# Kernel tuning notes

Hardware: AMD Instinct MI355X
Metric: run time of the kernel (lower is better)

Reference implementation:

```python
import jax, jax.numpy as jnp
import numpy as np
import math

D_MODEL, D_STATE, N_LAYERS, D_CONV, EXPAND = 64, 16, 2, 4, 2
D_INNER = EXPAND * D_MODEL
DT_RANK = math.ceil(D_MODEL / 16)
B, N, T = 2, 16, 2048


def setup_inputs() -> dict:
    key = jax.random.key(0)
    ks = jax.random.split(key, 10)
    A_row = jnp.log(jnp.arange(1, D_STATE + 1, dtype=jnp.float32))  # S4D-real init
    return {
        "x": jax.random.normal(ks[0], (B, N, T), jnp.float32),
        "input_proj_w": jax.random.normal(ks[1], (D_MODEL, 1), jnp.float32) * 0.02,
        "input_proj_b": jnp.zeros((D_MODEL,), jnp.float32),
        "in_proj_w": jax.random.normal(ks[2], (N_LAYERS, 2 * D_INNER, D_MODEL), jnp.float32) * 0.02,
        "conv_w": jax.random.normal(ks[3], (N_LAYERS, D_INNER, 1, D_CONV), jnp.float32) * 0.1,
        "conv_b": jnp.zeros((N_LAYERS, D_INNER), jnp.float32),
        "x_proj_w": jax.random.normal(ks[4], (N_LAYERS, DT_RANK + 2 * D_STATE, D_INNER), jnp.float32) * 0.02,
        "dt_proj_w": jax.random.normal(ks[5], (N_LAYERS, D_INNER, DT_RANK), jnp.float32) * 0.1,
        "dt_proj_b": jax.random.normal(ks[6], (N_LAYERS, D_INNER), jnp.float32) * 0.02,
        "A_log": jnp.tile(A_row[None, None, :], (N_LAYERS, D_INNER, 1)),  # [L, d_inner, d_state]
        "D": jnp.ones((N_LAYERS, D_INNER), jnp.float32),
        "out_proj_w": jax.random.normal(ks[7], (N_LAYERS, D_MODEL, D_INNER), jnp.float32) * 0.02,
    }


def _silu(v):
    return v * jax.nn.sigmoid(v)


def _mamba_block(h, in_w, cw, cb, xw, dtw, dtb, A_log, Dp, ow):
    # h: [Bf, T, d_model]
    xr = jnp.einsum('btd,ed->bte', h, in_w)           # [Bf, T, 2*d_inner]
    x, res = jnp.split(xr, 2, axis=-1)                # each [Bf, T, d_inner]
    # causal depthwise conv1d (torch: padding=d_conv-1 then truncate to T)
    xc = jnp.transpose(x, (0, 2, 1))                  # [Bf, d_inner, T]
    xc = jax.lax.conv_general_dilated(xc, cw, (1,), [(D_CONV - 1, 0)],
                                      feature_group_count=D_INNER)
    x = _silu(jnp.transpose(xc, (0, 2, 1)) + cb[None, None, :])
    A = -jnp.exp(A_log)                               # [d_inner, d_state]
    x_dbl = jnp.einsum('btd,ed->bte', x, xw)          # [Bf, T, dt_rank+2*d_state]
    delta, Bm, Cm = jnp.split(x_dbl, [DT_RANK, DT_RANK + D_STATE], axis=-1)
    delta = jax.nn.softplus(jnp.einsum('btr,dr->btd', delta, dtw) + dtb)

    def step(hs, inp):
        d_t, B_t, C_t, u_t = inp                      # [Bf,d], [Bf,n], [Bf,n], [Bf,d]
        dA = jnp.exp(d_t[:, :, None] * A)             # [Bf, d, n]
        hs = dA * hs + (d_t * u_t)[:, :, None] * B_t[:, None, :]
        return hs, jnp.einsum('bdn,bn->bd', hs, C_t)

    xs = (jnp.swapaxes(delta, 0, 1), jnp.swapaxes(Bm, 0, 1),
          jnp.swapaxes(Cm, 0, 1), jnp.swapaxes(x, 0, 1))
    hs0 = jnp.zeros((h.shape[0], D_INNER, D_STATE), h.dtype)
    _, ys = jax.lax.scan(step, hs0, xs)               # ys: [T, Bf, d_inner]
    y = jnp.swapaxes(ys, 0, 1) + x * Dp[None, None, :]
    y = y * _silu(res)
    return jnp.einsum('btd,md->btm', y, ow) + h       # block residual


def reference(x, input_proj_w, input_proj_b, in_proj_w, conv_w, conv_b,
              x_proj_w, dt_proj_w, dt_proj_b, A_log, D, out_proj_w):
    b, n, t = x.shape
    h = x.reshape(b * n, t, 1)
    h = jnp.einsum('btk,dk->btd', h, input_proj_w) + input_proj_b
    for l in range(N_LAYERS):
        h = _mamba_block(h, in_proj_w[l], conv_w[l], conv_b[l], x_proj_w[l],
                         dt_proj_w[l], dt_proj_b[l], A_log[l], D[l], out_proj_w[l])
    return h.reshape(b, n, t, D_MODEL)
```

## Files before the change

kernel.cpp:

```cpp
#include <hip/hip_runtime.h>
#include <hip/hip_bf16.h>

#define BN     32
#define T      2048
#define DM     64
#define DI     128
#define DS     16
#define DTR    4
#define NLAY   2
#define RTOT   (BN*T)
#define NC     128
#define LC     (T/NC)

typedef float v2f __attribute__((ext_vector_type(2)));
typedef float f32x4 __attribute__((ext_vector_type(4)));
typedef __bf16 bf16x8 __attribute__((ext_vector_type(8)));
struct V22 { v2f a, b; };

__device__ __forceinline__ float silu_f(float v) {
    return v / (1.f + __expf(-v));
}
__device__ __forceinline__ unsigned short f2bf(float f) {
    __hip_bfloat16 b = __float2bfloat16(f);
    return __builtin_bit_cast(unsigned short, b);
}
__device__ __forceinline__ float bf_lo(unsigned int u) { return __uint_as_float(u << 16); }
__device__ __forceinline__ float bf_hi(unsigned int u) { return __uint_as_float(u & 0xffff0000u); }
__device__ __forceinline__ float us2f(unsigned short u) { return __uint_as_float(((unsigned)u) << 16); }
__device__ __forceinline__ void f4v2(const float4 f, v2f& a, v2f& b) {
    V22 u = __builtin_bit_cast(V22, f);
    a = u.a; b = u.b;
}
__device__ __forceinline__ float4 v2f4(v2f a, v2f b) {
    V22 u; u.a = a; u.b = b;
    return __builtin_bit_cast(float4, u);
}
__device__ __forceinline__ f32x4 mfma16(bf16x8 a, bf16x8 b, f32x4 c) {
    return __builtin_amdgcn_mfma_f32_16x16x32_bf16(a, b, c, 0, 0, 0);
}

#define E_POWERS2(e1, EE)                                              \
    float p2 = (e1)*(e1); float p4 = p2*p2; float p8 = p4*p4;          \
    v2f EE[8];                                                         \
    EE[0] = (v2f){(e1), p2};                                           \
    EE[1] = EE[0] * p2;                                                \
    EE[2] = EE[0] * p4;                                                \
    EE[3] = EE[1] * p4;                                                \
    EE[4] = EE[0] * p8;                                                \
    EE[5] = EE[1] * p8;                                                \
    EE[6] = EE[2] * p8;                                                \
    EE[7] = EE[3] * p8;

__global__ void k_initwt(const float* __restrict__ inw, const float* __restrict__ xw,
                         const float* __restrict__ ow, unsigned short* __restrict__ wti,
                         unsigned short* __restrict__ wtx, unsigned short* __restrict__ wto) {
    int i = blockIdx.x * 256 + threadIdx.x;
    if (i < 32768) {
        int l = i >> 14, pos = i & 16383;
        int j    = pos & 7;
        int lane = (pos >> 3) & 63;
        int ks   = (pos >> 9) & 1;
        int ct   = pos >> 10;
        int e = ct * 16 + (lane & 15);
        int k = ks * 32 + ((lane >> 4) & 3) * 8 + j;
        wti[l * 16384 + pos] = f2bf(inw[l * 16384 + e * 64 + k]);
    } else if (i < 45056) {
        int j = i - 32768;
        int l = (j >= 6144) ? 1 : 0;
        int pos = j - l * 6144;
        int jj   = pos & 7;
        int lane = (pos >> 3) & 63;
        int ks   = (pos >> 9) & 3;
        int ct   = pos >> 11;
        int m = ct * 16 + (lane & 15);
        int k = ks * 32 + ((lane >> 4) & 3) * 8 + jj;
        wtx[l * 6144 + pos] = (m < 36) ? f2bf(xw[l * 4608 + m * 128 + k])
                                       : (unsigned short)0;
    } else if (i < 61440) {
        int j = i - 45056;
        int l = j >> 13, pos = j & 8191;
        int jj   = pos & 7;
        int lane = (pos >> 3) & 63;
        int ks   = (pos >> 9) & 3;
        int ct   = pos >> 11;
        int m = ct * 16 + (lane & 15);
        int k = ks * 32 + ((lane >> 4) & 3) * 8 + jj;
        wto[l * 8192 + pos] = f2bf(ow[l * 8192 + m * 128 + k]);
    }
}

__global__ __launch_bounds__(256, 4)
void k_inconv(const float* __restrict__ hg, const float* __restrict__ xin,
              const float* __restrict__ ipw, const float* __restrict__ ipb,
              float* __restrict__ hout, const int L0,
              const unsigned short* __restrict__ wtiF,
              const float* __restrict__ cw, const float* __restrict__ cb,
              const unsigned short* __restrict__ wtxF,
              const float* __restrict__ dtw, const float* __restrict__ dtb,
              unsigned short* __restrict__ ubf, unsigned short* __restrict__ rbf,
              unsigned short* __restrict__ Hp, float* __restrict__ Sd) {
    __shared__ __align__(16) float smem[10112];
    unsigned short* A16 = (unsigned short*)smem;
    unsigned short* xub = A16 + 11520;
    float* xdbf = smem;

    const int tid  = threadIdx.x;
    const int base = blockIdx.x * 64;
    const int t0   = base & (T - 1);

#pragma unroll
    for (int k5 = 0; k5 < 5; ++k5) {
        int s = tid + k5 * 256;
        int i = s >> 4, q = s & 15;
        int lt = t0 - 16 + i;
        float4 v = make_float4(0.f, 0.f, 0.f, 0.f);
        if (lt >= 0) {
            int row = base - 16 + i;
            if (L0) {
                float xv = xin[row];
                float4 wq = *(const float4*)&ipw[q * 4];
                float4 bq = *(const float4*)&ipb[q * 4];
                v = make_float4(xv * wq.x + bq.x, xv * wq.y + bq.y,
                                xv * wq.z + bq.z, xv * wq.w + bq.w);
                if (i >= 16) *(float4*)&hout[(size_t)row * 64 + q * 4] = v;
            } else {
                v = *(const float4*)&hg[(size_t)row * 64 + q * 4];
            }
        }
        float vf[4] = {v.x, v.y, v.z, v.w};
        unsigned short hs[4], ls[4];
#pragma unroll
        for (int m = 0; m < 4; ++m) {
            hs[m] = f2bf(vf[m]);
            float hf = us2f(hs[m]);
            ls[m] = f2bf(vf[m] - hf);
        }
        unsigned int hw0 = (unsigned)hs[0] | ((unsigned)hs[1] << 16);
        unsigned int hw1 = (unsigned)hs[2] | ((unsigned)hs[3] << 16);
        unsigned int lw0 = (unsigned)ls[0] | ((unsigned)ls[1] << 16);
        unsigned int lw1 = (unsigned)ls[2] | ((unsigned)ls[3] << 16);
        *(uint2*)&A16[(size_t)i * 72 + q * 4]        = make_uint2(hw0, hw1);
        *(uint2*)&A16[(size_t)(80 + i) * 72 + q * 4] = make_uint2(lw0, lw1);
    }

    const int l  = tid & 63;
    const int w  = tid >> 6;
    const int lr = l & 15;
    const int lg = l >> 4;

    const uint4* bp = (const uint4*)wtiF;
    bf16x8 bfr[4][2];
#pragma unroll
    for (int ct = 0; ct < 4; ++ct)
#pragma unroll
        for (int ks = 0; ks < 2; ++ks)
            bfr[ct][ks] = __builtin_bit_cast(bf16x8, bp[(((w * 4 + ct) * 2 + ks) * 64) + l]);

    __syncthreads();

    f32x4 acc[5][4];
#pragma unroll
    for (int rt = 0; rt < 5; ++rt)
#pragma unroll
        for (int ct = 0; ct < 4; ++ct)
            acc[rt][ct] = (f32x4){0.f, 0.f, 0.f, 0.f};

#pragma unroll
    for (int rt = 0; rt < 5; ++rt) {
        if (rt == 0 && w >= 2) continue;
        bf16x8 ah[2], al[2];
#pragma unroll
        for (int ks = 0; ks < 2; ++ks) {
            int idx = (rt * 16 + lr) * 72 + ks * 32 + lg * 8;
            ah[ks] = __builtin_bit_cast(bf16x8, *(const uint4*)&A16[idx]);
            al[ks] = __builtin_bit_cast(bf16x8, *(const uint4*)&A16[80 * 72 + idx]);
        }
#pragma unroll
        for (int ct = 0; ct < 4; ++ct) {
#pragma unroll
            for (int ks = 0; ks < 2; ++ks) {
                acc[rt][ct] = mfma16(ah[ks], bfr[ct][ks], acc[rt][ct]);
                acc[rt][ct] = mfma16(al[ks], bfr[ct][ks], acc[rt][ct]);
            }
        }
    }

    if (w < 2) {
        const int srcl = (l + 48) & 63;
        float4 cwv[4]; float cbv[4];
#pragma unroll
        for (int ct = 0; ct < 4; ++ct) {
            int c = w * 64 + ct * 16 + lr;
            cwv[ct] = *(const float4*)&cw[c * 4];
            cbv[ct] = cb[c];
        }
#pragma unroll
        for (int rt = 1; rt < 5; ++rt) {
#pragma unroll
            for (int ct = 0; ct < 4; ++ct) {
                float d1 = __shfl(acc[rt][ct][1], srcl);
                float d2 = __shfl(acc[rt][ct][2], srcl);
                float d3 = __shfl(acc[rt][ct][3], srcl);
                float p1 = __shfl(acc[rt - 1][ct][1], srcl);
                float p2 = __shfl(acc[rt - 1][ct][2], srcl);
                float p3 = __shfl(acc[rt - 1][ct][3], srcl);
                float m41 = (lg == 0) ? p1 : d1;
                float m42 = (lg == 0) ? p2 : d2;
                float m43 = (lg == 0) ? p3 : d3;
                float q0 = acc[rt][ct][0], q1 = acc[rt][ct][1];
                float q2 = acc[rt][ct][2], q3 = acc[rt][ct][3];
                float x3v[4] = {m41, m42, m43, q0};
                float x2v[4] = {m42, m43, q0, q1};
                float x1v[4] = {m43, q0, q1, q2};
                float x0v[4] = {q0, q1, q2, q3};
                int rb0 = (rt - 1) * 16 + lg * 4;
                int c = w * 64 + ct * 16 + lr;
#pragma unroll
                for (int rg = 0; rg < 4; ++rg) {
                    float v = cbv[ct] + cwv[ct].x * x3v[rg] + cwv[ct].y * x2v[rg]
                                      + cwv[ct].z * x1v[rg] + cwv[ct].w * x0v[rg];
                    xub[(rb0 + rg) * 136 + c] = f2bf(silu_f(v));
                }
            }
        }
    } else {
#pragma unroll
        for (int rt = 1; rt < 5; ++rt)
#pragma unroll
            for (int ct = 0; ct < 4; ++ct)
#pragma unroll
                for (int rg = 0; rg < 4; ++rg) {
                    int i = rt * 16 + lg * 4 + rg;
                    int row = base + i - 16;
                    int cR = (w - 2) * 64 + ct * 16 + lr;
                    rbf[(size_t)row * 128 + cR] = f2bf(acc[rt][ct][rg]);
                }
    }

    __syncthreads();

    {
        for (int idx = tid; idx < 512; idx += 256) {
            int r = idx >> 4, q = idx & 15;
            uint4 v = *(const uint4*)&xub[r * 136 + q * 8];
            *(uint4*)&ubf[(size_t)(base + r) * 128 + q * 8] = v;
        }
    }
    {
        bf16x8 bx[3][4];
        const uint4* xp = (const uint4*)wtxF;
#pragma unroll
        for (int ct = 0; ct < 3; ++ct)
#pragma unroll
            for (int ks = 0; ks < 4; ++ks)
                bx[ct][ks] = __builtin_bit_cast(bf16x8, xp[((ct * 4 + ks) * 64) + l]);
        bf16x8 a[4];
#pragma unroll
        for (int ks = 0; ks < 4; ++ks)
            a[ks] = __builtin_bit_cast(bf16x8,
                *(const uint4*)&xub[(w * 16 + lr) * 136 + ks * 32 + lg * 8]);
        f32x4 acx[3];
#pragma unroll
        for (int ct = 0; ct < 3; ++ct) acx[ct] = (f32x4){0.f, 0.f, 0.f, 0.f};
#pragma unroll
        for (int ct = 0; ct < 3; ++ct)
#pragma unroll
            for (int ks = 0; ks < 4; ++ks)
                acx[ct] = mfma16(a[ks], bx[ct][ks], acx[ct]);
#pragma unroll
        for (int ct = 0; ct < 3; ++ct) {
            int cA = ct * 16 + lr;
            if (cA < 36) {
#pragma unroll
                for (int rg = 0; rg < 4; ++rg)
                    xdbf[(w * 16 + lg * 4 + rg) * 40 + cA] = acx[ct][rg];
            }
        }
    }
    __syncthreads();

    {
        const int d  = tid & 127, cl = tid >> 7;
        const int s  = base >> 11;
        float4 dw = ((const float4*)dtw)[d];
        float db = dtb[d];
#pragma unroll
        for (int p = 0; p < 2; ++p) {
            const int rl0 = (p * 2 + cl) * 16;
            v2f hh2[8] = {};
            float sdsum = 0.f;
            float dvc, e1c;
            {
                const float* xd0 = &xdbf[rl0 * 40];
                float a0 = db + xd0[0]*dw.x + xd0[1]*dw.y + xd0[2]*dw.z + xd0[3]*dw.w;
                float ea0 = __expf(a0);
                dvc = (a0 > 20.f) ? a0 : __logf(1.f + ea0);
                e1c = __builtin_amdgcn_rcpf(1.f + ea0);
            }
            for (int t = 0; t < LC; t++) {
                int rl  = rl0 + t;
                int rln = rl0 + ((t + 1 < LC) ? t + 1 : t);
                const float* xdn = &xdbf[rln * 40];
                float an  = db + xdn[0]*dw.x + xdn[1]*dw.y + xdn[2]*dw.z + xdn[3]*dw.w;
                float ean = __expf(an);
                float dvn = (an > 20.f) ? an : __logf(1.f + ean);
                float e1n = __builtin_amdgcn_rcpf(1.f + ean);
                float uv = us2f(xub[rl * 136 + d]);
                float du = dvc * uv;
                sdsum += dvc;
                E_POWERS2(e1c, ee2)
                const float4* bq = (const float4*)&xdbf[rl * 40 + 4];
                v2f Bv[8];
                f4v2(bq[0], Bv[0], Bv[1]); f4v2(bq[1], Bv[2], Bv[3]);
                f4v2(bq[2], Bv[4], Bv[5]); f4v2(bq[3], Bv[6], Bv[7]);
#pragma unroll
                for (int n = 0; n < 8; n++) hh2[n] = ee2[n] * hh2[n] + Bv[n] * du;
                dvc = dvn; e1c = e1n;
            }
            int cg = (t0 >> 4) + p * 2 + cl;
            size_t o = ((size_t)cg * 4096 + (size_t)(s * 128 + d)) * 16;
            unsigned int hw[8];
#pragma unroll
            for (int i = 0; i < 8; i++)
                hw[i] = (unsigned)f2bf(hh2[i].x) | ((unsigned)f2bf(hh2[i].y) << 16);
            *(uint4*)&Hp[o]     = make_uint4(hw[0], hw[1], hw[2], hw[3]);
            *(uint4*)&Hp[o + 8] = make_uint4(hw[4], hw[5], hw[6], hw[7]);
            Sd[cg * 4096 + s * 128 + d] = sdsum;
        }
    }
}

__global__ __launch_bounds__(256, 8)
void k_scan2(const float* __restrict__ Alog, const float* __restrict__ Sd,
             unsigned short* __restrict__ Hp) {
    int g = blockIdx.x * 256 + threadIdx.x;
    int n = g & 15, sdi = g >> 4;
    float An = -__expf(Alog[(sdi & 127) * 16 + n]);
    float cur = 0.f;
    float sdb[8]; unsigned short hpb[8];
#pragma unroll
    for (int j = 0; j < 8; ++j) {
        sdb[j] = Sd[j * 4096 + sdi];
        hpb[j] = Hp[((size_t)j * 4096 + sdi) * 16 + n];
    }
    for (int cb = 0; cb < NC / 8; ++cb) {
        float sdn[8] = {};
        unsigned short hpn[8] = {};
        if (cb + 1 < NC / 8) {
#pragma unroll
            for (int j = 0; j < 8; ++j) {
                int c = (cb + 1) * 8 + j;
                sdn[j] = Sd[c * 4096 + sdi];
                hpn[j] = Hp[((size_t)c * 4096 + sdi) * 16 + n];
            }
        }
#pragma unroll
        for (int j = 0; j < 8; ++j) {
            int c = cb * 8 + j;
            size_t idx = ((size_t)c * 4096 + sdi) * 16 + n;
            float hp_c = us2f(hpb[j]);
            Hp[idx] = f2bf(cur);
            cur = hp_c + __expf(An * sdb[j]) * cur;
        }
#pragma unroll
        for (int j = 0; j < 8; ++j) { sdb[j] = sdn[j]; hpb[j] = hpn[j]; }
    }
}

__global__ __launch_bounds__(256, 7)
void k_scan3out(const unsigned short* __restrict__ ubf, const unsigned short* __restrict__ rbf,
                const unsigned short* __restrict__ wtxF,
                const float* __restrict__ dtw, const float* __restrict__ dtb,
                const float* __restrict__ Dp, const unsigned short* __restrict__ hin,
                const unsigned short* __restrict__ wto, float* __restrict__ h) {
    __shared__ __align__(16) unsigned short xub[32 * 136];
    __shared__ __align__(16) float xdb[32 * 40];
    __shared__ __align__(16) unsigned short yls[32 * 136];
    const int blk = blockIdx.x;
    const int s = blk >> 6, cp = blk & 63;
    const int tid = threadIdx.x;
    const int rowb = s * T + cp * 32;
    {
        const uint4* src = (const uint4*)(ubf + (size_t)rowb * 128);
        for (int idx = tid; idx < 512; idx += 256) {
            int r = idx >> 4, q = idx & 15;
            *(uint4*)&xub[r * 136 + q * 8] = src[idx];
        }
    }
    const int l  = tid & 63, w = tid >> 6;
    const int lr = l & 15,  lg = l >> 4;
    const int rt  = w & 1;
    const int ctA = (w < 2) ? 0 : 2;
    bf16x8 bfrA[4], bfrB[4];
    {
        const uint4* bp = (const uint4*)wtxF;
#pragma unroll
        for (int ks = 0; ks < 4; ++ks)
            bfrA[ks] = __builtin_bit_cast(bf16x8, bp[((ctA * 4 + ks) * 64) + l]);
        if (w < 2) {
#pragma unroll
            for (int ks = 0; ks < 4; ++ks)
                bfrB[ks] = __builtin_bit_cast(bf16x8, bp[((4 + ks) * 64) + l]);
        }
    }
    __syncthreads();
    {
        bf16x8 a[4];
#pragma unroll
        for (int ks = 0; ks < 4; ++ks)
            a[ks] = __builtin_bit_cast(bf16x8,
                *(const uint4*)&xub[(rt * 16 + lr) * 136 + ks * 32 + lg * 8]);
        f32x4 accA = (f32x4){0.f, 0.f, 0.f, 0.f};
        f32x4 accB = (f32x4){0.f, 0.f, 0.f, 0.f};
#pragma unroll
        for (int ks = 0; ks < 4; ++ks) accA = mfma16(a[ks], bfrA[ks], accA);
        if (w < 2) {
#pragma unroll
            for (int ks = 0; ks < 4; ++ks) accB = mfma16(a[ks], bfrB[ks], accB);
        }
        int cA = ctA * 16 + lr;
        if (cA < 36) {
#pragma unroll
            for (int rg = 0; rg < 4; ++rg)
                xdb[(rt * 16 + lg * 4 + rg) * 40 + cA] = accA[rg];
        }
        if (w < 2) {
#pragma unroll
            for (int rg = 0; rg < 4; ++rg)
                xdb[(rt * 16 + lg * 4 + rg) * 40 + 16 + lr] = accB[rg];
        }
    }
    __syncthreads();
    {
        const int d = tid & 127, ci = tid >> 7;
        const int c = cp * 2 + ci;
        const float Dd = Dp[d];
        float4 dw4 = ((const float4*)dtw)[d];
        float db = dtb[d];
        size_t o = ((size_t)c * 4096 + (size_t)(s * 128 + d)) * 16;
        const uint4* hp4 = (const uint4*)&hin[o];
        uint4 ha = hp4[0], hb = hp4[1];
        v2f hh2[8];
        hh2[0] = (v2f){bf_lo(ha.x), bf_hi(ha.x)};
        hh2[1] = (v2f){bf_lo(ha.y), bf_hi(ha.y)};
        hh2[2] = (v2f){bf_lo(ha.z), bf_hi(ha.z)};
        hh2[3] = (v2f){bf_lo(ha.w), bf_hi(ha.w)};
        hh2[4] = (v2f){bf_lo(hb.x), bf_hi(hb.x)};
        hh2[5] = (v2f){bf_lo(hb.y), bf_hi(hb.y)};
        hh2[6] = (v2f){bf_lo(hb.z), bf_hi(hb.z)};
        hh2[7] = (v2f){bf_lo(hb.w), bf_hi(hb.w)};
        size_t rof = (size_t)(rowb + ci * 16) * 128 + d;
        const unsigned short* rp = rbf + rof;
        const int lb = ci * 16;
        float rv = us2f(rp[0]);
        float dvc, e1c;
        {
            const float* xd0 = &xdb[lb * 40];
            float a0 = db + xd0[0]*dw4.x + xd0[1]*dw4.y + xd0[2]*dw4.z + xd0[3]*dw4.w;
            float ea0 = __expf(a0);
            dvc = (a0 > 20.f) ? a0 : __logf(1.f + ea0);
            e1c = __builtin_amdgcn_rcpf(1.f + ea0);
        }
        for (int t = 0; t < LC; t++) {
            int tn = (t + 1 < LC) ? t + 1 : t;
            float rvn = us2f(rp[tn * 128]);
            const float* xdn = &xdb[(lb + tn) * 40];
            float an  = db + xdn[0]*dw4.x + xdn[1]*dw4.y + xdn[2]*dw4.z + xdn[3]*dw4.w;
            float ean = __expf(an);
            float dvn = (an > 20.f) ? an : __logf(1.f + ean);
            float e1n = __builtin_amdgcn_rcpf(1.f + ean);
            float uv = us2f(xub[(lb + t) * 136 + d]);
            float du = dvc * uv;
            E_POWERS2(e1c, ee2)
            const float* xd = &xdb[(lb + t) * 40];
            const float4* bq = (const float4*)&xd[4];
            const float4* cq = (const float4*)&xd[20];
            v2f Bv[8], Cv[8];
            f4v2(bq[0], Bv[0], Bv[1]); f4v2(bq[1], Bv[2], Bv[3]);
            f4v2(bq[2], Bv[4], Bv[5]); f4v2(bq[3], Bv[6], Bv[7]);
            f4v2(cq[0], Cv[0], Cv[1]); f4v2(cq[1], Cv[2], Cv[3]);
            f4v2(cq[2], Cv[4], Cv[5]); f4v2(cq[3], Cv[6], Cv[7]);
            v2f yac = (v2f){0.f, 0.f};
#pragma unroll
            for (int n = 0; n < 8; n++) {
                hh2[n] = ee2[n] * hh2[n] + Bv[n] * du;
                yac += hh2[n] * Cv[n];
            }
            float y = yac.x + yac.y;
            yls[(lb + t) * 136 + d] = f2bf((y + uv * Dd) * silu_f(rv));
            rv = rvn; dvc = dvn; e1c = e1n;
        }
    }
    __syncthreads();
    float* outb = (float*)yls;
    {
        const int cp2 = w >> 1;
        bf16x8 bfo[2][4];
        {
            const uint4* op = (const uint4*)wto;
#pragma unroll
            for (int cc = 0; cc < 2; ++cc)
#pragma unroll
                for (int ks = 0; ks < 4; ++ks) {
                    int ct = cp2 * 2 + cc;
                    bfo[cc][ks] = __builtin_bit_cast(bf16x8, op[((ct * 4 + ks) * 64) + l]);
                }
        }
        bf16x8 a[4];
#pragma unroll
        for (int ks = 0; ks < 4; ++ks)
            a[ks] = __builtin_bit_cast(bf16x8,
                *(const uint4*)&yls[(rt * 16 + lr) * 136 + ks * 32 + lg * 8]);
        f32x4 acc[2];
        acc[0] = (f32x4){0.f, 0.f, 0.f, 0.f};
        acc[1] = (f32x4){0.f, 0.f, 0.f, 0.f};
#pragma unroll
        for (int ks = 0; ks < 4; ++ks) {
            acc[0] = mfma16(a[ks], bfo[0][ks], acc[0]);
            acc[1] = mfma16(a[ks], bfo[1][ks], acc[1]);
        }
        __syncthreads();
#pragma unroll
        for (int cc = 0; cc < 2; ++cc) {
            int m = cp2 * 32 + cc * 16 + lr;
#pragma unroll
            for (int rg = 0; rg < 4; ++rg)
                outb[(rt * 16 + lg * 4 + rg) * 68 + m] = acc[cc][rg];
        }
    }
    __syncthreads();
    {
        const int r = tid >> 3, cg = tid & 7;
        size_t o = (size_t)(rowb + r) * 64 + cg * 8;
        float4 h0 = *(const float4*)&h[o];
        float4 h1 = *(const float4*)&h[o + 4];
        float4 o0 = *(const float4*)&outb[r * 68 + cg * 8];
        float4 o1 = *(const float4*)&outb[r * 68 + cg * 8 + 4];
        h0.x += o0.x; h0.y += o0.y; h0.z += o0.z; h0.w += o0.w;
        h1.x += o1.x; h1.y += o1.y; h1.z += o1.z; h1.w += o1.w;
        *(float4*)&h[o]     = h0;
        *(float4*)&h[o + 4] = h1;
    }
}

extern "C" void kernel_launch(void* const* d_in, const int* in_sizes, int n_in,
                              void* d_out, int out_size, void* d_ws, size_t ws_size,
                              hipStream_t stream) {
    (void)in_sizes; (void)n_in; (void)out_size; (void)ws_size;
    const float* x    = (const float*)d_in[0];
    const float* ipw  = (const float*)d_in[1];
    const float* ipb  = (const float*)d_in[2];
    const float* inw  = (const float*)d_in[3];
    const float* cw   = (const float*)d_in[4];
    const float* cb   = (const float*)d_in[5];
    const float* xw   = (const float*)d_in[6];
    const float* dtw  = (const float*)d_in[7];
    const float* dtb  = (const float*)d_in[8];
    const float* Alog = (const float*)d_in[9];
    const float* Dp   = (const float*)d_in[10];
    const float* ow   = (const float*)d_in[11];
    float* h = (float*)d_out;

    unsigned short* ubf = (unsigned short*)d_ws;
    unsigned short* rbf = ubf + 8388608;
    unsigned short* Hpb = rbf + 8388608;
    float* Sdb    = (float*)(Hpb + (size_t)NC * 65536);
    unsigned short* wti = (unsigned short*)(Sdb + (size_t)NC * 4096);
    unsigned short* wtx = wti + 32768;
    unsigned short* wto = wtx + 12288;

    k_initwt<<<240, 256, 0, stream>>>(inw, xw, ow, wti, wtx, wto);
    for (int l = 0; l < NLAY; l++) {
        k_inconv<<<RTOT / 64, 256, 0, stream>>>(h, x, ipw, ipb, h, (l == 0) ? 1 : 0,
                                                wti + l * 16384,
                                                cw + l * 128 * 4, cb + l * 128,
                                                wtx + l * 6144,
                                                dtw + l * 128 * 4, dtb + l * 128,
                                                ubf, rbf, Hpb, Sdb);
        k_scan2<<<256, 256, 0, stream>>>(Alog + l * 128 * 16, Sdb, Hpb);
        k_scan3out<<<2048, 256, 0, stream>>>(ubf, rbf, wtx + l * 6144,
                                             dtw + l * 128 * 4, dtb + l * 128,
                                             Dp + l * 128, Hpb, wto + l * 8192, h);
    }
}
```

Measured before the change: 233.6 us.

## Fold input projection into layer-0 in_proj as rank-1 weights, skip MFMA

For the first layer the hidden state is an affine function of a scalar input, so in_proj(h) equals x*(W·ipw) + W·ipb. The weight-prep kernel now precomputes these two 256-vectors, and layer 0 of k_inconv computes the conv and residual paths directly from the scalar input instead of staging bf16 hi/lo tiles and running MFMAs. This removes the layer-0 GEMM and its shared-memory staging. It also changes numerics slightly, since the fp32 products replace the split-bf16 GEMM, and adds a small serial dot-product loop to the init kernel.

```diff
diff --git a/kernel.cpp b/kernel.cpp
--- a/kernel.cpp
+++ b/kernel.cpp
@@ -52,8 +52,10 @@
     EE[7] = EE[3] * p8;
 
 __global__ void k_initwt(const float* __restrict__ inw, const float* __restrict__ xw,
-                         const float* __restrict__ ow, unsigned short* __restrict__ wti,
-                         unsigned short* __restrict__ wtx, unsigned short* __restrict__ wto) {
+                         const float* __restrict__ ow, const float* __restrict__ ipw,
+                         const float* __restrict__ ipb, unsigned short* __restrict__ wti,
+                         unsigned short* __restrict__ wtx, unsigned short* __restrict__ wto,
+                         float* __restrict__ w1b1) {
     int i = blockIdx.x * 256 + threadIdx.x;
     if (i < 32768) {
         int l = i >> 14, pos = i & 16383;
@@ -86,12 +88,20 @@
         int m = ct * 16 + (lane & 15);
         int k = ks * 32 + ((lane >> 4) & 3) * 8 + jj;
         wto[l * 8192 + pos] = f2bf(ow[l * 8192 + m * 128 + k]);
+    } else if (i < 61952) {
+        int e = i - 61440;
+        const float* vec = (e < 256) ? ipw : ipb;
+        int c = e & 255;
+        float s = 0.f;
+        for (int k = 0; k < 64; ++k) s += inw[c * 64 + k] * vec[k];
+        w1b1[e] = s;
     }
 }
 
 __global__ __launch_bounds__(256, 4)
 void k_inconv(const float* __restrict__ hg, const float* __restrict__ xin,
               const float* __restrict__ ipw, const float* __restrict__ ipb,
+              const float* __restrict__ w1b1,
               float* __restrict__ hout, const int L0,
               const unsigned short* __restrict__ wtiF,
               const float* __restrict__ cw, const float* __restrict__ cb,
@@ -103,138 +113,196 @@
     unsigned short* A16 = (unsigned short*)smem;
     unsigned short* xub = A16 + 11520;
     float* xdbf = smem;
+    float* wb   = smem + 4000;
 
     const int tid  = threadIdx.x;
     const int base = blockIdx.x * 64;
     const int t0   = base & (T - 1);
-
-#pragma unroll
-    for (int k5 = 0; k5 < 5; ++k5) {
-        int s = tid + k5 * 256;
-        int i = s >> 4, q = s & 15;
-        int lt = t0 - 16 + i;
-        float4 v = make_float4(0.f, 0.f, 0.f, 0.f);
-        if (lt >= 0) {
-            int row = base - 16 + i;
-            if (L0) {
-                float xv = xin[row];
-                float4 wq = *(const float4*)&ipw[q * 4];
-                float4 bq = *(const float4*)&ipb[q * 4];
-                v = make_float4(xv * wq.x + bq.x, xv * wq.y + bq.y,
-                                xv * wq.z + bq.z, xv * wq.w + bq.w);
-                if (i >= 16) *(float4*)&hout[(size_t)row * 64 + q * 4] = v;
-            } else {
-                v = *(const float4*)&hg[(size_t)row * 64 + q * 4];
-            }
-        }
-        float vf[4] = {v.x, v.y, v.z, v.w};
-        unsigned short hs[4], ls[4];
-#pragma unroll
-        for (int m = 0; m < 4; ++m) {
-            hs[m] = f2bf(vf[m]);
-            float hf = us2f(hs[m]);
-            ls[m] = f2bf(vf[m] - hf);
-        }
-        unsigned int hw0 = (unsigned)hs[0] | ((unsigned)hs[1] << 16);
-        unsigned int hw1 = (unsigned)hs[2] | ((unsigned)hs[3] << 16);
-        unsigned int lw0 = (unsigned)ls[0] | ((unsigned)ls[1] << 16);
-        unsigned int lw1 = (unsigned)ls[2] | ((unsigned)ls[3] << 16);
-        *(uint2*)&A16[(size_t)i * 72 + q * 4]        = make_uint2(hw0, hw1);
-        *(uint2*)&A16[(size_t)(80 + i) * 72 + q * 4] = make_uint2(lw0, lw1);
-    }
 
     const int l  = tid & 63;
     const int w  = tid >> 6;
     const int lr = l & 15;
     const int lg = l >> 4;
 
-    const uint4* bp = (const uint4*)wtiF;
     bf16x8 bfr[4][2];
-#pragma unroll
-    for (int ct = 0; ct < 4; ++ct)
-#pragma unroll
-        for (int ks = 0; ks < 2; ++ks)
-            bfr[ct][ks] = __builtin_bit_cast(bf16x8, bp[(((w * 4 + ct) * 2 + ks) * 64) + l]);
+
+    if (L0) {
+#pragma unroll
+        for (int it = 0; it < 4; ++it) {
+            int s = tid + it * 256;
+            int r = s >> 4, q = s & 15;
+            float xv = xin[base + r];
+            float4 wq = *(const float4*)&ipw[q * 4];
+            float4 bq = *(const float4*)&ipb[q * 4];
+            float4 v = make_float4(xv * wq.x + bq.x, xv * wq.y + bq.y,
+                                   xv * wq.z + bq.z, xv * wq.w + bq.w);
+            *(float4*)&hout[(size_t)(base + r) * 64 + q * 4] = v;
+        }
+        wb[tid]       = w1b1[tid];
+        wb[256 + tid] = w1b1[256 + tid];
+    } else {
+#pragma unroll
+        for (int k5 = 0; k5 < 5; ++k5) {
+            int s = tid + k5 * 256;
+            int i = s >> 4, q = s & 15;
+            int lt = t0 - 16 + i;
+            float4 v = make_float4(0.f, 0.f, 0.f, 0.f);
+            if (lt >= 0) v = *(const float4*)&hg[(size_t)(base - 16 + i) * 64 + q * 4];
+            float vf[4] = {v.x, v.y, v.z, v.w};
+            unsigned short hs[4], ls[4];
+#pragma unroll
+            for (int m = 0; m < 4; ++m) {
+                hs[m] = f2bf(vf[m]);
+                float hf = us2f(hs[m]);
+                ls[m] = f2bf(vf[m] - hf);
+            }
+            unsigned int hw0 = (unsigned)hs[0] | ((unsigned)hs[1] << 16);
+            unsigned int hw1 = (unsigned)hs[2] | ((unsigned)hs[3] << 16);
+            unsigned int lw0 = (unsigned)ls[0] | ((unsigned)ls[1] << 16);
+            unsigned int lw1 = (unsigned)ls[2] | ((unsigned)ls[3] << 16);
+            *(uint2*)&A16[(size_t)i * 72 + q * 4]        = make_uint2(hw0, hw1);
+            *(uint2*)&A16[(size_t)(80 + i) * 72 + q * 4] = make_uint2(lw0, lw1);
+        }
+        const uint4* bp = (const uint4*)wtiF;
+#pragma unroll
+        for (int ct = 0; ct < 4; ++ct)
+#pragma unroll
+            for (int ks = 0; ks < 2; ++ks)
+                bfr[ct][ks] = __builtin_bit_cast(bf16x8, bp[(((w * 4 + ct) * 2 + ks) * 64) + l]);
+    }
 
     __syncthreads();
 
-    f32x4 acc[5][4];
-#pragma unroll
-    for (int rt = 0; rt < 5; ++rt)
-#pragma unroll
-        for (int ct = 0; ct < 4; ++ct)
-            acc[rt][ct] = (f32x4){0.f, 0.f, 0.f, 0.f};
-
-#pragma unroll
-    for (int rt = 0; rt < 5; ++rt) {
-        if (rt == 0 && w >= 2) continue;
-        bf16x8 ah[2], al[2];
-#pragma unroll
-        for (int ks = 0; ks < 2; ++ks) {
-            int idx = (rt * 16 + lr) * 72 + ks * 32 + lg * 8;
-            ah[ks] = __builtin_bit_cast(bf16x8, *(const uint4*)&A16[idx]);
-            al[ks] = __builtin_bit_cast(bf16x8, *(const uint4*)&A16[80 * 72 + idx]);
-        }
-#pragma unroll
-        for (int ct = 0; ct < 4; ++ct) {
+    if (L0) {
+        const int r  = tid >> 2;
+        const int cq = tid & 3;
+        const int c0 = cq * 32;
+        float xr4[4], sel4[4];
+#pragma unroll
+        for (int j = 0; j < 4; ++j) {
+            int lt = t0 + r - 3 + j;
+            bool ok = (lt >= 0);
+            xr4[j]  = ok ? xin[base + r - 3 + j] : 0.f;
+            sel4[j] = ok ? 1.f : 0.f;
+        }
+#pragma unroll
+        for (int q = 0; q < 8; ++q) {
+            int c = c0 + q * 4;
+            float4 w1q = *(const float4*)&wb[c];
+            float4 b1q = *(const float4*)&wb[256 + c];
+            float w1a[4] = {w1q.x, w1q.y, w1q.z, w1q.w};
+            float b1a[4] = {b1q.x, b1q.y, b1q.z, b1q.w};
+            float o[4];
+#pragma unroll
+            for (int m = 0; m < 4; ++m) {
+                float4 cwv = *(const float4*)&cw[(c + m) * 4];
+                float v0 = xr4[0] * w1a[m] + sel4[0] * b1a[m];
+                float v1 = xr4[1] * w1a[m] + sel4[1] * b1a[m];
+                float v2 = xr4[2] * w1a[m] + sel4[2] * b1a[m];
+                float v3 = xr4[3] * w1a[m] + sel4[3] * b1a[m];
+                float v = cb[c + m] + cwv.x * v0 + cwv.y * v1
+                                    + cwv.z * v2 + cwv.w * v3;
+                o[m] = silu_f(v);
+            }
+            unsigned int lo = (unsigned)f2bf(o[0]) | ((unsigned)f2bf(o[1]) << 16);
+            unsigned int hi = (unsigned)f2bf(o[2]) | ((unsigned)f2bf(o[3]) << 16);
+            *(uint2*)&xub[r * 136 + c] = make_uint2(lo, hi);
+        }
+        {
+            float xv = xr4[3];
+#pragma unroll
+            for (int q = 0; q < 8; ++q) {
+                int c = c0 + q * 4;
+                float4 w1q = *(const float4*)&wb[128 + c];
+                float4 b1q = *(const float4*)&wb[384 + c];
+                float o0 = xv * w1q.x + b1q.x;
+                float o1 = xv * w1q.y + b1q.y;
+                float o2 = xv * w1q.z + b1q.z;
+                float o3 = xv * w1q.w + b1q.w;
+                unsigned int lo = (unsigned)f2bf(o0) | ((unsigned)f2bf(o1) << 16);
+                unsigned int hi = (unsigned)f2bf(o2) | ((unsigned)f2bf(o3) << 16);
+                *(uint2*)&rbf[(size_t)(base + r) * 128 + c] = make_uint2(lo, hi);
+            }
+        }
+    } else {
+        f32x4 acc[5][4];
+#pragma unroll
+        for (int rt = 0; rt < 5; ++rt)
+#pragma unroll
+            for (int ct = 0; ct < 4; ++ct)
+                acc[rt][ct] = (f32x4){0.f, 0.f, 0.f, 0.f};
+
+#pragma unroll
+        for (int rt = 0; rt < 5; ++rt) {
+            if (rt == 0 && w >= 2) continue;
+            bf16x8 ah[2], al[2];
 #pragma unroll
             for (int ks = 0; ks < 2; ++ks) {
-                acc[rt][ct] = mfma16(ah[ks], bfr[ct][ks], acc[rt][ct]);
-                acc[rt][ct] = mfma16(al[ks], bfr[ct][ks], acc[rt][ct]);
-            }
-        }
-    }
-
-    if (w < 2) {
-        const int srcl = (l + 48) & 63;
-        float4 cwv[4]; float cbv[4];
-#pragma unroll
-        for (int ct = 0; ct < 4; ++ct) {
-            int c = w * 64 + ct * 16 + lr;
-            cwv[ct] = *(const float4*)&cw[c * 4];
-            cbv[ct] = cb[c];
-        }
-#pragma unroll
-        for (int rt = 1; rt < 5; ++rt) {
+                int idx = (rt * 16 + lr) * 72 + ks * 32 + lg * 8;
+                ah[ks] = __builtin_bit_cast(bf16x8, *(const uint4*)&A16[idx]);
+                al[ks] = __builtin_bit_cast(bf16x8, *(const uint4*)&A16[80 * 72 + idx]);
+            }
 #pragma unroll
             for (int ct = 0; ct < 4; ++ct) {
-                float d1 = __shfl(acc[rt][ct][1], srcl);
-                float d2 = __shfl(acc[rt][ct][2], srcl);
-                float d3 = __shfl(acc[rt][ct][3], srcl);
-                float p1 = __shfl(acc[rt - 1][ct][1], srcl);
-                float p2 = __shfl(acc[rt - 1][ct][2], srcl);
-                float p3 = __shfl(acc[rt - 1][ct][3], srcl);
-                float m41 = (lg == 0) ? p1 : d1;
-                float m42 = (lg == 0) ? p2 : d2;
-                float m43 = (lg == 0) ? p3 : d3;
-                float q0 = acc[rt][ct][0], q1 = acc[rt][ct][1];
-                float q2 = acc[rt][ct][2], q3 = acc[rt][ct][3];
-                float x3v[4] = {m41, m42, m43, q0};
-                float x2v[4] = {m42, m43, q0, q1};
-                float x1v[4] = {m43, q0, q1, q2};
-                float x0v[4] = {q0, q1, q2, q3};
-                int rb0 = (rt - 1) * 16 + lg * 4;
+#pragma unroll
+                for (int ks = 0; ks < 2; ++ks) {
+                    acc[rt][ct] = mfma16(ah[ks], bfr[ct][ks], acc[rt][ct]);
+                    acc[rt][ct] = mfma16(al[ks], bfr[ct][ks], acc[rt][ct]);
+                }
+            }
+        }
+
+        if (w < 2) {
+            const int srcl = (l + 48) & 63;
+            float4 cwv[4]; float cbv[4];
+#pragma unroll
+            for (int ct = 0; ct < 4; ++ct) {
                 int c = w * 64 + ct * 16 + lr;
-#pragma unroll
-                for (int rg = 0; rg < 4; ++rg) {
-                    float v = cbv[ct] + cwv[ct].x * x3v[rg] + cwv[ct].y * x2v[rg]
-                                      + cwv[ct].z * x1v[rg] + cwv[ct].w * x0v[rg];
-                    xub[(rb0 + rg) * 136 + c] = f2bf(silu_f(v));
+                cwv[ct] = *(const float4*)&cw[c * 4];
+                cbv[ct] = cb[c];
+            }
+#pragma unroll
+            for (int rt = 1; rt < 5; ++rt) {
+#pragma unroll
+                for (int ct = 0; ct < 4; ++ct) {
+                    float d1 = __shfl(acc[rt][ct][1], srcl);
+                    float d2 = __shfl(acc[rt][ct][2], srcl);
+                    float d3 = __shfl(acc[rt][ct][3], srcl);
+                    float p1 = __shfl(acc[rt - 1][ct][1], srcl);
+                    float p2 = __shfl(acc[rt - 1][ct][2], srcl);
+                    float p3 = __shfl(acc[rt - 1][ct][3], srcl);
+                    float m41 = (lg == 0) ? p1 : d1;
+                    float m42 = (lg == 0) ? p2 : d2;
+                    float m43 = (lg == 0) ? p3 : d3;
+                    float q0 = acc[rt][ct][0], q1 = acc[rt][ct][1];
+                    float q2 = acc[rt][ct][2], q3 = acc[rt][ct][3];
+                    float x3v[4] = {m41, m42, m43, q0};
+                    float x2v[4] = {m42, m43, q0, q1};
+                    float x1v[4] = {m43, q0, q1, q2};
+                    float x0v[4] = {q0, q1, q2, q3};
+                    int rb0 = (rt - 1) * 16 + lg * 4;
+                    int c = w * 64 + ct * 16 + lr;
+#pragma unroll
+                    for (int rg = 0; rg < 4; ++rg) {
+                        float v = cbv[ct] + cwv[ct].x * x3v[rg] + cwv[ct].y * x2v[rg]
+                                          + cwv[ct].z * x1v[rg] + cwv[ct].w * x0v[rg];
+                        xub[(rb0 + rg) * 136 + c] = f2bf(silu_f(v));
+                    }
                 }
             }
-        }
-    } else {
-#pragma unroll
-        for (int rt = 1; rt < 5; ++rt)
-#pragma unroll
-            for (int ct = 0; ct < 4; ++ct)
-#pragma unroll
-                for (int rg = 0; rg < 4; ++rg) {
-                    int i = rt * 16 + lg * 4 + rg;
-                    int row = base + i - 16;
-                    int cR = (w - 2) * 64 + ct * 16 + lr;
-                    rbf[(size_t)row * 128 + cR] = f2bf(acc[rt][ct][rg]);
-                }
+        } else {
+#pragma unroll
+            for (int rt = 1; rt < 5; ++rt)
+#pragma unroll
+                for (int ct = 0; ct < 4; ++ct)
+#pragma unroll
+                    for (int rg = 0; rg < 4; ++rg) {
+                        int i = rt * 16 + lg * 4 + rg;
+                        int row = base + i - 16;
+                        int cR = (w - 2) * 64 + ct * 16 + lr;
+                        rbf[(size_t)row * 128 + cR] = f2bf(acc[rt][ct][rg]);
+                    }
+        }
     }
 
     __syncthreads();
@@ -568,10 +636,11 @@
     unsigned short* wti = (unsigned short*)(Sdb + (size_t)NC * 4096);
     unsigned short* wtx = wti + 32768;
     unsigned short* wto = wtx + 12288;
-
-    k_initwt<<<240, 256, 0, stream>>>(inw, xw, ow, wti, wtx, wto);
+    float* w1b1 = (float*)(wto + 16384);
+
+    k_initwt<<<242, 256, 0, stream>>>(inw, xw, ow, ipw, ipb, wti, wtx, wto, w1b1);
     for (int l = 0; l < NLAY; l++) {
-        k_inconv<<<RTOT / 64, 256, 0, stream>>>(h, x, ipw, ipb, h, (l == 0) ? 1 : 0,
+        k_inconv<<<RTOT / 64, 256, 0, stream>>>(h, x, ipw, ipb, w1b1, h, (l == 0) ? 1 : 0,
                                                 wti + l * 16384,
                                                 cw + l * 128 * 4, cb + l * 128,
                                                 wtx + l * 6144,
```

New measurement: 249.3 us. +6.7%, slower.
